# Kernel tuning notes

Hardware: AMD Instinct MI355X
Metric: run time of the kernel (lower is better)

The kernel has to match this reference:

```python
import jax, jax.numpy as jnp
import numpy as np

C = 256
LN_EPS = 1e-5

def setup_inputs() -> dict:
    key = jax.random.key(0)
    ks = jax.random.split(key, 12)
    B, M, N = 8, 4096, 4096
    scale = 1.0 / np.sqrt(C)
    inp = {
        'x': jax.random.normal(ks[0], (B, M, C), jnp.float32),
        'y': jax.random.normal(ks[1], (B, N, C), jnp.float32),
        'Wq': jax.random.normal(ks[2], (C, C), jnp.float32) * scale,
        'bq': jnp.zeros((C,), jnp.float32),
        'Wk': jax.random.normal(ks[3], (C, C), jnp.float32) * scale,
        'bk': jnp.zeros((C,), jnp.float32),
        'Wv': jax.random.normal(ks[4], (C, C), jnp.float32) * scale,
        'bv': jnp.zeros((C,), jnp.float32),
        'Wo': jax.random.normal(ks[5], (C, C), jnp.float32) * (scale * 1e-5),
        'bo': jnp.zeros((C,), jnp.float32),
        'gamma': jnp.ones((C,), jnp.float32),
        'beta': jnp.zeros((C,), jnp.float32),
    }
    return inp

def reference(x, y, Wq, bq, Wk, bk, Wv, bv, Wo, bo, gamma, beta):
    # projections (torch Linear: x @ W.T + b)
    q = x @ Wq.T + bq                      # [B,M,C]
    k = y @ Wk.T + bk                      # [B,N,C]
    v = y @ Wv.T + bv                      # [B,N,C]
    # scaled dot-product attention with explicit score matrix
    w = jnp.einsum('bmc,bnc->bmn', q, k) * (C ** -0.5)  # [B,M,N]
    w = jax.nn.softmax(w, axis=-1)
    h = jnp.einsum('bmn,bnc->bmc', w, v)   # [B,M,C]
    h = h @ Wo.T + bo
    z = x + h
    # LayerNorm over last dim
    mu = jnp.mean(z, axis=-1, keepdims=True)
    var = jnp.var(z, axis=-1, keepdims=True)
    out = (z - mu) * jax.lax.rsqrt(var + LN_EPS) * gamma + beta
    return out
```

## Files before the change

kernel.cpp:

```cpp
#include <hip/hip_runtime.h>
#include <hip/hip_bf16.h>

#define C_DIM 256
#define QSCALE 0.09016844f
#define WO_SCALE 1048576.0f
#define WO_INV   9.5367431640625e-07f

typedef __attribute__((ext_vector_type(8))) short bf16x8;
typedef __attribute__((ext_vector_type(4))) float f32x4;
typedef __attribute__((ext_vector_type(16))) float f32x16;

__device__ __forceinline__ void gload16(const unsigned char* g, unsigned char* l) {
    __builtin_amdgcn_global_load_lds(
        (const __attribute__((address_space(1))) void*)g,
        (__attribute__((address_space(3))) void*)l, 16, 0, 0);
}

__global__ void cvt_w_kernel(const float* __restrict__ w0, const float* __restrict__ w1,
                             const float* __restrict__ w2, const float* __restrict__ w3,
                             unsigned char* __restrict__ o0, unsigned char* __restrict__ o1,
                             unsigned char* __restrict__ o2, unsigned char* __restrict__ o3) {
    int i = (blockIdx.x * 256 + threadIdx.x) * 4;
    #pragma unroll
    for (int wsel = 0; wsel < 4; ++wsel) {
        const float* w = wsel == 0 ? w0 : (wsel == 1 ? w1 : (wsel == 2 ? w2 : w3));
        unsigned char* o = wsel == 0 ? o0 : (wsel == 1 ? o1 : (wsel == 2 ? o2 : o3));
        const float sc = (wsel == 3) ? WO_SCALE : 1.0f;
        float4 v = *reinterpret_cast<const float4*>(w + i);
        unsigned p = __builtin_amdgcn_cvt_pk_fp8_f32(v.x * sc, v.y * sc, 0, false);
        p = __builtin_amdgcn_cvt_pk_fp8_f32(v.z * sc, v.w * sc, p, true);
        *reinterpret_cast<unsigned*>(o + i) = p;
    }
}

__global__ __launch_bounds__(256, 1)
void proj_kernel(const float* __restrict__ x, const float* __restrict__ y,
                 const unsigned char* __restrict__ wq8, const unsigned char* __restrict__ wk8,
                 const unsigned char* __restrict__ wv8,
                 const float* __restrict__ bqp, const float* __restrict__ bkp,
                 const float* __restrict__ bvp,
                 unsigned char* __restrict__ qo, unsigned char* __restrict__ ko,
                 unsigned char* __restrict__ vo)
{
    __shared__ __align__(16) unsigned char ldsW[65536];
    __shared__ __align__(16) unsigned char ldsA[32768];

    const int which = blockIdx.x >> 8;
    const int tile = blockIdx.x & 255;
    const float* in = (which == 0) ? x : y;
    const unsigned char* wsrc = (which == 0) ? wq8 : (which == 1 ? wk8 : wv8);
    const float* bias = (which == 0) ? bqp : (which == 1 ? bkp : bvp);
    unsigned char* out = (which == 0) ? qo : (which == 1 ? ko : vo);
    const float oscale = (which == 0) ? QSCALE : 1.0f;

    const int tid = threadIdx.x;
    const int rowbase = tile * 128;

    #pragma unroll
    for (int it = 0; it < 16; ++it) {
        int G = it * 256 + tid;
        int c = G >> 4, p = G & 15;
        gload16(wsrc + c * 256 + ((p ^ (c & 15)) << 4), ldsW + G * 16);
    }
    #pragma unroll
    for (int it = 0; it < 32; ++it) {
        int e = it * 1024 + tid * 4;
        int r = e >> 8, c4 = e & 255;
        float4 v = *reinterpret_cast<const float4*>(in + (size_t)(rowbase + r) * C_DIM + c4);
        unsigned p = __builtin_amdgcn_cvt_pk_fp8_f32(v.x, v.y, 0, false);
        p = __builtin_amdgcn_cvt_pk_fp8_f32(v.z, v.w, p, true);
        int g = (c4 >> 4) ^ (r & 15);
        *reinterpret_cast<unsigned*>(ldsA + r * 256 + g * 16 + (c4 & 12)) = p;
    }
    __syncthreads();

    const int lane = tid & 63, wave = tid >> 6;
    const int lrow = lane & 15, lkq = lane >> 4;
    const int koff = (lkq & 1) << 3;
    const int kg = lkq >> 1;

    #pragma unroll
    for (int ms = 0; ms < 2; ++ms) {
        const int arow = wave * 32 + ms * 16 + lrow;
        long a[8];
        #pragma unroll
        for (int ks = 0; ks < 8; ++ks)
            a[ks] = *reinterpret_cast<const long*>(
                ldsA + arow * 256 + (((ks * 2 + kg) ^ (arow & 15)) << 4) + koff);

        f32x4 acc[16];
        #pragma unroll
        for (int nf = 0; nf < 16; ++nf) acc[nf] = f32x4{0.f, 0.f, 0.f, 0.f};

        #pragma unroll
        for (int nf = 0; nf < 16; ++nf) {
            const int c = nf * 16 + lrow;
            const unsigned char* wb = ldsW + c * 256;
            const int cx = c & 15;
            #pragma unroll
            for (int ks = 0; ks < 8; ++ks) {
                long b = *reinterpret_cast<const long*>(wb + (((ks * 2 + kg) ^ cx) << 4) + koff);
                acc[nf] = __builtin_amdgcn_mfma_f32_16x16x32_fp8_fp8(a[ks], b, acc[nf], 0, 0, 0);
            }
        }

        const int base = rowbase + wave * 32 + ms * 16 + lkq * 4;
        if (which != 2) {
            const int rsw = (which == 1) ? (base & 8) : 0;
            #pragma unroll
            for (int nf = 0; nf < 16; ++nf) {
                float bv = bias[nf * 16 + lrow];
                float v0 = (acc[nf][0] + bv) * oscale, v1 = (acc[nf][1] + bv) * oscale;
                float v2 = (acc[nf][2] + bv) * oscale, v3 = (acc[nf][3] + bv) * oscale;
                unsigned p = __builtin_amdgcn_cvt_pk_fp8_f32(v0, v1, 0, false);
                p = __builtin_amdgcn_cvt_pk_fp8_f32(v2, v3, p, true);
                int col = (nf * 16 + lrow) ^ rsw;
                unsigned char* o = out + (size_t)base * C_DIM + col;
                o[0]   = (unsigned char)p;
                o[256] = (unsigned char)(p >> 8);
                o[512] = (unsigned char)(p >> 16);
                o[768] = (unsigned char)(p >> 24);
            }
        } else {
            int bb = base >> 12, n0 = base & 4095;
            #pragma unroll
            for (int nf = 0; nf < 16; ++nf) {
                float bv = bias[nf * 16 + lrow];
                float v0 = acc[nf][0] + bv, v1 = acc[nf][1] + bv;
                float v2 = acc[nf][2] + bv, v3 = acc[nf][3] + bv;
                unsigned p = __builtin_amdgcn_cvt_pk_fp8_f32(v0, v1, 0, false);
                p = __builtin_amdgcn_cvt_pk_fp8_f32(v2, v3, p, true);
                int c = nf * 16 + lrow;
                *reinterpret_cast<unsigned*>(vo + ((size_t)bb * C_DIM + c) * 4096 + (n0 ^ (c & 8))) = p;
            }
        }
    }
}

__global__ __launch_bounds__(512, 1)
void attn_kernel(const unsigned char* __restrict__ qg, const unsigned char* __restrict__ kg,
                 const unsigned char* __restrict__ vtg, unsigned short* __restrict__ hg)
{
    __shared__ __align__(16) unsigned short smem[65536];
    unsigned char* smb = (unsigned char*)smem;

    const int tid = threadIdx.x;
    const int lane = tid & 63;
    const int w = tid >> 6;
    const int wq = w & 3;
    const int half = w >> 2;
    const int l31 = lane & 31;
    const int hi5 = lane >> 5;
    const int ksw = l31 & 15;
    const int hsw = ((l31 >> 3) & 1) << 3;
    const int vsw = ((l31 >> 2) & 1);

    const int batch = blockIdx.x & 7;
    const int mt = blockIdx.x >> 3;
    const size_t q0 = (size_t)batch * 4096 + mt * 128 + wq * 32;

    const unsigned char* kbase = kg + ((size_t)batch * 4096 + half * 2048) * 256;
    const unsigned char* vbase = vtg + (size_t)batch * 256 * 4096 + half * 2048;

    long qf[16];
    #pragma unroll
    for (int ks = 0; ks < 16; ++ks)
        qf[ks] = *reinterpret_cast<const long*>(qg + (q0 + l31) * 256 + ks * 16 + hi5 * 8);

    f32x16 o[8];
    #pragma unroll
    for (int cb = 0; cb < 8; ++cb) {
        #pragma unroll
        for (int r = 0; r < 16; ++r) o[cb][r] = 0.f;
    }

    float m_run = -__builtin_inff();
    float lsum = 0.f;

    auto stage = [&](int buf, int kt) {
        const int kv0 = kt * 32;
        unsigned char* lk = smb + (half * 2 + buf) * 8192;
        unsigned char* lv = smb + 32768 + (half * 2 + buf) * 8192;
        #pragma unroll
        for (int i = 0; i < 2; ++i) {
            int g = wq * 128 + i * 64 + lane;
            int row = g >> 4, pos = g & 15;
            gload16(kbase + (size_t)(kv0 + row) * 256 + ((pos ^ (row & 15)) << 4), lk + g * 16);
        }
        #pragma unroll
        for (int i = 0; i < 2; ++i) {
            int s = wq * 128 + i * 64 + lane;
            int c = s >> 1;
            int k2 = (s & 1) ^ ((s >> 3) & 1);
            gload16(vbase + (size_t)c * 4096 + kv0 + k2 * 16, lv + s * 16);
        }
    };

    stage(0, 0);
    __syncthreads();

    for (int kt = 0; kt < 64; ++kt) {
        const int cur = kt & 1;
        if (kt < 63) stage(cur ^ 1, kt + 1);

        const unsigned char* kc = smb + (half * 2 + cur) * 8192;
        const unsigned char* vc = smb + 32768 + (half * 2 + cur) * 8192;

        f32x16 s0;
        #pragma unroll
        for (int r = 0; r < 16; ++r) s0[r] = 0.f;
        const unsigned char* krow = kc + l31 * 256 + ((hi5 * 8) ^ hsw);
        __builtin_amdgcn_s_setprio(1);
        #pragma unroll
        for (int ks = 0; ks < 16; ++ks) {
            long a0 = *reinterpret_cast<const long*>(krow + ((ks ^ ksw) << 4));
            s0 = __builtin_amdgcn_mfma_f32_32x32x16_fp8_fp8(a0, qf[ks], s0, 0, 0, 0);
        }
        __builtin_amdgcn_s_setprio(0);

        float mloc = s0[0];
        #pragma unroll
        for (int r = 1; r < 16; ++r) mloc = fmaxf(mloc, s0[r]);
        mloc = fmaxf(mloc, __shfl_xor(mloc, 32, 64));

        if (__any(mloc > m_run + 8.0f)) {
            float mn = fmaxf(m_run, mloc);
            float al = exp2f(m_run - mn);
            m_run = mn;
            lsum *= al;
            #pragma unroll
            for (int cb = 0; cb < 8; ++cb) {
                #pragma unroll
                for (int r = 0; r < 16; ++r) o[cb][r] *= al;
            }
        }

        float ts = 0.f;
        #pragma unroll
        for (int r = 0; r < 16; ++r) { s0[r] = exp2f(s0[r] - m_run); ts += s0[r]; }
        ts += __shfl_xor(ts, 32, 64);
        lsum += ts;

        unsigned Wu[8];
        #pragma unroll
        for (int a = 0; a < 8; ++a) {
            unsigned p = __builtin_amdgcn_cvt_pk_fp8_f32(s0[4 * a], s0[4 * a + 1], 0, false);
            Wu[a] = __builtin_amdgcn_cvt_pk_fp8_f32(s0[4 * a + 2], s0[4 * a + 3], p, true);
        }

        const bool h = (hi5 != 0);
        const unsigned char* vrow = vc + l31 * 32 + ((hi5 * 8) ^ hsw);
        __builtin_amdgcn_s_setprio(1);
        #pragma unroll
        for (int ksv = 0; ksv < 2; ++ksv) {
            unsigned snd = h ? Wu[2 * ksv] : Wu[2 * ksv + 1];
            unsigned rcv = __shfl_xor(snd, 32, 64);
            unsigned wlo = h ? rcv : Wu[2 * ksv];
            unsigned whi = h ? Wu[2 * ksv + 1] : rcv;
            long pb = (long)(((unsigned long long)whi << 32) | (unsigned long long)wlo);
            const int k2s = (ksv ^ vsw) << 4;
            #pragma unroll
            for (int cb = 0; cb < 8; ++cb) {
                long vf = *reinterpret_cast<const long*>(vrow + cb * 1024 + k2s);
                o[cb] = __builtin_amdgcn_mfma_f32_32x32x16_fp8_fp8(vf, pb, o[cb], 0, 0, 0);
            }
        }
        __builtin_amdgcn_s_setprio(0);

        __syncthreads();
    }

    float* sf = (float*)smem;

    if (half == 1 && hi5 == 0) {
        sf[(wq * 32 + l31) * 2]     = m_run;
        sf[(wq * 32 + l31) * 2 + 1] = lsum;
    }
    __syncthreads();

    float m1 = 0.f, l1 = 0.f;
    if (half == 0) {
        m1 = sf[(wq * 32 + l31) * 2];
        l1 = sf[(wq * 32 + l31) * 2 + 1];
    }
    __syncthreads();

    if (half == 1) {
        #pragma unroll
        for (int cb = 0; cb < 8; ++cb) {
            #pragma unroll
            for (int r = 0; r < 16; ++r) {
                int c = cb * 32 + (r & 3) + 8 * (r >> 2) + 4 * hi5;
                sf[wq * 8192 + c * 32 + l31] = o[cb][r];
            }
        }
    }
    __syncthreads();

    if (half == 0) {
        float mm = fmaxf(m_run, m1);
        float a0 = exp2f(m_run - mm), a1 = exp2f(m1 - mm);
        float lt = lsum * a0 + l1 * a1;
        float rinv = 1.0f / lt;
        float f0 = a0 * rinv, f1 = a1 * rinv;

        unsigned short* tr = smem + wq * 16384;
        #pragma unroll
        for (int cc = 0; cc < 4; ++cc) {
            #pragma unroll
            for (int cbh = 0; cbh < 2; ++cbh) {
                const int cb = cc * 2 + cbh;
                #pragma unroll
                for (int rp = 0; rp < 8; ++rp) {
                    const int r = 2 * rp;
                    int c_lo = cb * 32 + (r & 3) + 8 * (r >> 2) + 4 * hi5;
                    float v_lo = o[cb][r]     * f0 + sf[wq * 8192 + c_lo * 32 + l31]       * f1;
                    float v_hi = o[cb][r + 1] * f0 + sf[wq * 8192 + (c_lo + 1) * 32 + l31] * f1;
                    unsigned wpk;
                    asm("v_cvt_pk_bf16_f32 %0, %1, %2" : "=v"(wpk) : "v"(v_lo), "v"(v_hi));
                    int c_local = 32 * cbh + (r & 3) + 8 * (r >> 2) + 4 * hi5;
                    *reinterpret_cast<unsigned*>(tr + l31 * 72 + c_local) = wpk;
                }
            }
            __builtin_amdgcn_s_waitcnt(0);
            #pragma unroll
            for (int i = 0; i < 4; ++i) {
                int idx = i * 64 + lane;
                int q = idx >> 3, ch = idx & 7;
                uint4 d = *reinterpret_cast<const uint4*>(tr + q * 72 + ch * 8);
                *reinterpret_cast<uint4*>(hg + (q0 + q) * 256 + cc * 64 + ch * 8) = d;
            }
        }
    }
}

__global__ __launch_bounds__(256, 1)
void out_kernel(const unsigned short* __restrict__ hb, const unsigned char* __restrict__ wo8,
                const float* __restrict__ bo, const float* __restrict__ xg,
                const float* __restrict__ gamma, const float* __restrict__ beta,
                float* __restrict__ outg)
{
    __shared__ __align__(16) unsigned char ldsW[65536];
    __shared__ __align__(16) unsigned char ldsA[32768];

    const int tid = threadIdx.x;
    const int rowbase = blockIdx.x * 128;

    #pragma unroll
    for (int it = 0; it < 16; ++it) {
        int G = it * 256 + tid;
        int c = G >> 4, p = G & 15;
        gload16(wo8 + c * 256 + ((p ^ (c & 15)) << 4), ldsW + G * 16);
    }
    #pragma unroll
    for (int it = 0; it < 16; ++it) {
        int e = it * 2048 + tid * 8;
        int r = e >> 8, c8 = e & 255;
        uint4 d = *reinterpret_cast<const uint4*>(hb + (size_t)(rowbase + r) * C_DIM + c8);
        union { unsigned u; float f; } f0, f1, f2, f3, f4, f5, f6, f7;
        f0.u = d.x << 16; f1.u = d.x & 0xffff0000u;
        f2.u = d.y << 16; f3.u = d.y & 0xffff0000u;
        f4.u = d.z << 16; f5.u = d.z & 0xffff0000u;
        f6.u = d.w << 16; f7.u = d.w & 0xffff0000u;
        unsigned p0 = __builtin_amdgcn_cvt_pk_fp8_f32(f0.f, f1.f, 0, false);
        p0 = __builtin_amdgcn_cvt_pk_fp8_f32(f2.f, f3.f, p0, true);
        unsigned p1 = __builtin_amdgcn_cvt_pk_fp8_f32(f4.f, f5.f, 0, false);
        p1 = __builtin_amdgcn_cvt_pk_fp8_f32(f6.f, f7.f, p1, true);
        int g = (c8 >> 4) ^ (r & 15);
        uint2 pk; pk.x = p0; pk.y = p1;
        *reinterpret_cast<uint2*>(ldsA + r * 256 + g * 16 + (c8 & 8)) = pk;
    }
    __syncthreads();

    const int lane = tid & 63, wave = tid >> 6;
    const int lrow = lane & 15, lkq = lane >> 4;
    const int koff = (lkq & 1) << 3;
    const int kg = lkq >> 1;

    #pragma unroll
    for (int ms = 0; ms < 2; ++ms) {
        const int arow = wave * 32 + ms * 16 + lrow;
        long a[8];
        #pragma unroll
        for (int ks = 0; ks < 8; ++ks)
            a[ks] = *reinterpret_cast<const long*>(
                ldsA + arow * 256 + (((ks * 2 + kg) ^ (arow & 15)) << 4) + koff);

        f32x4 acc[16];
        #pragma unroll
        for (int nf = 0; nf < 16; ++nf) acc[nf] = f32x4{0.f, 0.f, 0.f, 0.f};

        #pragma unroll
        for (int nf = 0; nf < 16; ++nf) {
            const int c = nf * 16 + lrow;
            const unsigned char* wb = ldsW + c * 256;
            const int cx = c & 15;
            #pragma unroll
            for (int ks = 0; ks < 8; ++ks) {
                long b = *reinterpret_cast<const long*>(wb + (((ks * 2 + kg) ^ cx) << 4) + koff);
                acc[nf] = __builtin_amdgcn_mfma_f32_16x16x32_fp8_fp8(a[ks], b, acc[nf], 0, 0, 0);
            }
        }

        const int base = rowbase + wave * 32 + ms * 16 + lkq * 4;

        #pragma unroll
        for (int nf = 0; nf < 16; ++nf) {
            float bv = bo[nf * 16 + lrow];
            #pragma unroll
            for (int r = 0; r < 4; ++r) {
                size_t row = base + r;
                acc[nf][r] = acc[nf][r] * WO_INV + bv + xg[row * C_DIM + nf * 16 + lrow];
            }
        }

        float mu[4], rstd[4];
        #pragma unroll
        for (int r = 0; r < 4; ++r) {
            float s1 = 0.f, s2 = 0.f;
            #pragma unroll
            for (int nf = 0; nf < 16; ++nf) { float v = acc[nf][r]; s1 += v; s2 += v * v; }
            #pragma unroll
            for (int off = 1; off < 16; off <<= 1) {
                s1 += __shfl_xor(s1, off, 64);
                s2 += __shfl_xor(s2, off, 64);
            }
            float m = s1 * (1.f / 256.f);
            mu[r] = m;
            rstd[r] = rsqrtf(s2 * (1.f / 256.f) - m * m + 1e-5f);
        }

        #pragma unroll
        for (int nf = 0; nf < 16; ++nf) {
            float g = gamma[nf * 16 + lrow];
            float bt = beta[nf * 16 + lrow];
            #pragma unroll
            for (int r = 0; r < 4; ++r) {
                size_t row = base + r;
                outg[row * C_DIM + nf * 16 + lrow] = (acc[nf][r] - mu[r]) * rstd[r] * g + bt;
            }
        }
    }
}

extern "C" void kernel_launch(void* const* d_in, const int* in_sizes, int n_in,
                              void* d_out, int out_size, void* d_ws, size_t ws_size,
                              hipStream_t stream) {
    const float* x     = (const float*)d_in[0];
    const float* y     = (const float*)d_in[1];
    const float* Wq    = (const float*)d_in[2];
    const float* bq    = (const float*)d_in[3];
    const float* Wk    = (const float*)d_in[4];
    const float* bk    = (const float*)d_in[5];
    const float* Wv    = (const float*)d_in[6];
    const float* bv    = (const float*)d_in[7];
    const float* Wo    = (const float*)d_in[8];
    const float* bo    = (const float*)d_in[9];
    const float* gamma = (const float*)d_in[10];
    const float* beta  = (const float*)d_in[11];
    float* out = (float*)d_out;

    unsigned char* ws = (unsigned char*)d_ws;
    unsigned char* wq8 = ws;
    unsigned char* wk8 = ws + 65536;
    unsigned char* wv8 = ws + 131072;
    unsigned char* wo8 = ws + 196608;
    unsigned char* q_b = ws + 262144;
    unsigned char* k_b = q_b + 8388608;
    unsigned char* v_b = k_b + 8388608;
    unsigned short* h_b = (unsigned short*)(v_b + 8388608);

    cvt_w_kernel<<<64, 256, 0, stream>>>(Wq, Wk, Wv, Wo, wq8, wk8, wv8, wo8);

    proj_kernel<<<768, 256, 0, stream>>>(x, y, wq8, wk8, wv8, bq, bk, bv, q_b, k_b, v_b);

    attn_kernel<<<256, 512, 0, stream>>>(q_b, k_b, v_b, h_b);

    out_kernel<<<256, 256, 0, stream>>>(h_b, wo8, bo, x, gamma, beta, out);
}
```

Baseline: 184.6 us.

## Skew softmax/PV phase in second wave group and triple-buffer V tiles

The KV-split attention kernel now runs a software-pipelined schedule in the second half of the waves: each iteration does the softmax and PV for the previous tile before the QK^T MFMAs for the current tile. The aim is to stagger the two halves so their MFMA and VALU/exp phases overlap on the SIMDs. V gets three LDS buffers to support the one-tile lag, which grows shared memory to 96KB. The cross-half partial output is now passed through LDS as swizzled bf16 instead of fp32, cutting LDS traffic at the cost of some precision in the merge.

```diff
diff --git a/kernel.cpp b/kernel.cpp
--- a/kernel.cpp
+++ b/kernel.cpp
@@ -141,8 +141,7 @@
 void attn_kernel(const unsigned char* __restrict__ qg, const unsigned char* __restrict__ kg,
                  const unsigned char* __restrict__ vtg, unsigned short* __restrict__ hg)
 {
-    __shared__ __align__(16) unsigned short smem[65536];
-    unsigned char* smb = (unsigned char*)smem;
+    __shared__ __align__(16) unsigned char smb[98304];
 
     const int tid = threadIdx.x;
     const int lane = tid & 63;
@@ -177,10 +176,10 @@
     float m_run = -__builtin_inff();
     float lsum = 0.f;
 
-    auto stage = [&](int buf, int kt) {
+    auto stage = [&](int kb, int vb, int kt) {
         const int kv0 = kt * 32;
-        unsigned char* lk = smb + (half * 2 + buf) * 8192;
-        unsigned char* lv = smb + 32768 + (half * 2 + buf) * 8192;
+        unsigned char* lk = smb + (half * 2 + kb) * 8192;
+        unsigned char* lv = smb + 32768 + (half * 3 + vb) * 8192;
         #pragma unroll
         for (int i = 0; i < 2; ++i) {
             int g = wq * 128 + i * 64 + lane;
@@ -196,31 +195,23 @@
         }
     };
 
-    stage(0, 0);
-    __syncthreads();
-
-    for (int kt = 0; kt < 64; ++kt) {
-        const int cur = kt & 1;
-        if (kt < 63) stage(cur ^ 1, kt + 1);
-
-        const unsigned char* kc = smb + (half * 2 + cur) * 8192;
-        const unsigned char* vc = smb + 32768 + (half * 2 + cur) * 8192;
-
-        f32x16 s0;
-        #pragma unroll
-        for (int r = 0; r < 16; ++r) s0[r] = 0.f;
-        const unsigned char* krow = kc + l31 * 256 + ((hi5 * 8) ^ hsw);
+    auto do_S = [&](int kb, f32x16& sreg) {
+        const unsigned char* krow = smb + (half * 2 + kb) * 8192 + l31 * 256 + ((hi5 * 8) ^ hsw);
+        #pragma unroll
+        for (int r = 0; r < 16; ++r) sreg[r] = 0.f;
         __builtin_amdgcn_s_setprio(1);
         #pragma unroll
         for (int ks = 0; ks < 16; ++ks) {
             long a0 = *reinterpret_cast<const long*>(krow + ((ks ^ ksw) << 4));
-            s0 = __builtin_amdgcn_mfma_f32_32x32x16_fp8_fp8(a0, qf[ks], s0, 0, 0, 0);
+            sreg = __builtin_amdgcn_mfma_f32_32x32x16_fp8_fp8(a0, qf[ks], sreg, 0, 0, 0);
         }
         __builtin_amdgcn_s_setprio(0);
-
-        float mloc = s0[0];
-        #pragma unroll
-        for (int r = 1; r < 16; ++r) mloc = fmaxf(mloc, s0[r]);
+    };
+
+    auto do_SMPV = [&](f32x16& sreg, int vb) {
+        float mloc = sreg[0];
+        #pragma unroll
+        for (int r = 1; r < 16; ++r) mloc = fmaxf(mloc, sreg[r]);
         mloc = fmaxf(mloc, __shfl_xor(mloc, 32, 64));
 
         if (__any(mloc > m_run + 8.0f)) {
@@ -237,19 +228,20 @@
 
         float ts = 0.f;
         #pragma unroll
-        for (int r = 0; r < 16; ++r) { s0[r] = exp2f(s0[r] - m_run); ts += s0[r]; }
+        for (int r = 0; r < 16; ++r) { sreg[r] = exp2f(sreg[r] - m_run); ts += sreg[r]; }
         ts += __shfl_xor(ts, 32, 64);
         lsum += ts;
 
         unsigned Wu[8];
         #pragma unroll
         for (int a = 0; a < 8; ++a) {
-            unsigned p = __builtin_amdgcn_cvt_pk_fp8_f32(s0[4 * a], s0[4 * a + 1], 0, false);
-            Wu[a] = __builtin_amdgcn_cvt_pk_fp8_f32(s0[4 * a + 2], s0[4 * a + 3], p, true);
+            unsigned p = __builtin_amdgcn_cvt_pk_fp8_f32(sreg[4 * a], sreg[4 * a + 1], 0, false);
+            Wu[a] = __builtin_amdgcn_cvt_pk_fp8_f32(sreg[4 * a + 2], sreg[4 * a + 3], p, true);
         }
 
         const bool h = (hi5 != 0);
-        const unsigned char* vrow = vc + l31 * 32 + ((hi5 * 8) ^ hsw);
+        const unsigned char* vrow = smb + 32768 + (half * 3 + vb) * 8192
+                                    + l31 * 32 + ((hi5 * 8) ^ hsw);
         __builtin_amdgcn_s_setprio(1);
         #pragma unroll
         for (int ksv = 0; ksv < 2; ++ksv) {
@@ -266,45 +258,72 @@
             }
         }
         __builtin_amdgcn_s_setprio(0);
-
-        __syncthreads();
-    }
-
-    float* sf = (float*)smem;
-
-    if (half == 1 && hi5 == 0) {
-        sf[(wq * 32 + l31) * 2]     = m_run;
-        sf[(wq * 32 + l31) * 2 + 1] = lsum;
-    }
+    };
+
+    stage(0, 0, 0);
     __syncthreads();
 
-    float m1 = 0.f, l1 = 0.f;
+    f32x16 s0;
     if (half == 0) {
-        m1 = sf[(wq * 32 + l31) * 2];
-        l1 = sf[(wq * 32 + l31) * 2 + 1];
-    }
+        int vcur = 0, vnxt = 1;
+        for (int kt = 0; kt < 64; ++kt) {
+            if (kt < 63) stage((kt + 1) & 1, vnxt, kt + 1);
+            do_S(kt & 1, s0);
+            do_SMPV(s0, vcur);
+            __syncthreads();
+            vcur = vnxt; vnxt = (vnxt == 2) ? 0 : vnxt + 1;
+        }
+    } else {
+        int vprv = 2, vcur = 0, vnxt = 1;
+        for (int kt = 0; kt < 64; ++kt) {
+            if (kt < 63) stage((kt + 1) & 1, vnxt, kt + 1);
+            if (kt > 0) do_SMPV(s0, vprv);
+            do_S(kt & 1, s0);
+            __syncthreads();
+            vprv = vcur; vcur = vnxt; vnxt = (vnxt == 2) ? 0 : vnxt + 1;
+        }
+        do_SMPV(s0, vprv);
+    }
+
     __syncthreads();
 
+    unsigned short* pub = (unsigned short*)smb;
+    float* ml = (float*)(smb + 90112);
+
     if (half == 1) {
+        if (hi5 == 0) {
+            ml[(wq * 32 + l31) * 2]     = m_run;
+            ml[(wq * 32 + l31) * 2 + 1] = lsum;
+        }
+        unsigned short* prow = pub + (wq * 32 + l31) * 256;
+        const int cxor = (l31 & 15) << 2;
         #pragma unroll
         for (int cb = 0; cb < 8; ++cb) {
             #pragma unroll
-            for (int r = 0; r < 16; ++r) {
+            for (int rp = 0; rp < 8; ++rp) {
+                const int r = 2 * rp;
+                unsigned wpk;
+                float lo = o[cb][r], hi_ = o[cb][r + 1];
+                asm("v_cvt_pk_bf16_f32 %0, %1, %2" : "=v"(wpk) : "v"(lo), "v"(hi_));
                 int c = cb * 32 + (r & 3) + 8 * (r >> 2) + 4 * hi5;
-                sf[wq * 8192 + c * 32 + l31] = o[cb][r];
+                *reinterpret_cast<unsigned*>(prow + (c ^ cxor)) = wpk;
             }
         }
     }
     __syncthreads();
 
     if (half == 0) {
+        float m1 = ml[(wq * 32 + l31) * 2];
+        float l1 = ml[(wq * 32 + l31) * 2 + 1];
         float mm = fmaxf(m_run, m1);
         float a0 = exp2f(m_run - mm), a1 = exp2f(m1 - mm);
         float lt = lsum * a0 + l1 * a1;
         float rinv = 1.0f / lt;
         float f0 = a0 * rinv, f1 = a1 * rinv;
 
-        unsigned short* tr = smem + wq * 16384;
+        const unsigned short* prow = pub + (wq * 32 + l31) * 256;
+        const int cxor = (l31 & 15) << 2;
+        unsigned short* tr = (unsigned short*)(smb + 65536 + wq * 4608);
         #pragma unroll
         for (int cc = 0; cc < 4; ++cc) {
             #pragma unroll
@@ -313,9 +332,12 @@
                 #pragma unroll
                 for (int rp = 0; rp < 8; ++rp) {
                     const int r = 2 * rp;
-                    int c_lo = cb * 32 + (r & 3) + 8 * (r >> 2) + 4 * hi5;
-                    float v_lo = o[cb][r]     * f0 + sf[wq * 8192 + c_lo * 32 + l31]       * f1;
-                    float v_hi = o[cb][r + 1] * f0 + sf[wq * 8192 + (c_lo + 1) * 32 + l31] * f1;
+                    int c = cb * 32 + (r & 3) + 8 * (r >> 2) + 4 * hi5;
+                    unsigned pk = *reinterpret_cast<const unsigned*>(prow + (c ^ cxor));
+                    union { unsigned u; float f; } b0, b1;
+                    b0.u = pk << 16; b1.u = pk & 0xffff0000u;
+                    float v_lo = o[cb][r]     * f0 + b0.f * f1;
+                    float v_hi = o[cb][r + 1] * f0 + b1.f * f1;
                     unsigned wpk;
                     asm("v_cvt_pk_bf16_f32 %0, %1, %2" : "=v"(wpk) : "v"(v_lo), "v"(v_hi));
                     int c_local = 32 * cbh + (r & 3) + 8 * (r >> 2) + 4 * hi5;
```

Result: slower. 196.3 us (+6.3%).

## Split attention columns across waves with rotating single-wave softmax via LDS

Applied to the files above, without the earlier changes.

Reworks the attention kernel so each 256-thread block owns 32 query rows and each wave owns a 64-column slice of the output. One wave per KV tile, chosen round-robin, computes scores and the online softmax, then writes P and the rescale factors to LDS for all waves to use in the PV MFMAs. This cuts accumulator registers per wave, allowing four blocks per CU and removing the two-half merge at the end. In exchange, the score/softmax stage is serialized on one wave per tile and two block barriers are added per tile.

```diff
diff --git a/kernel.cpp b/kernel.cpp
--- a/kernel.cpp
+++ b/kernel.cpp
@@ -137,18 +137,15 @@
     }
 }
 
-__global__ __launch_bounds__(512, 1)
+__global__ __launch_bounds__(256, 4)
 void attn_kernel(const unsigned char* __restrict__ qg, const unsigned char* __restrict__ kg,
                  const unsigned char* __restrict__ vtg, unsigned short* __restrict__ hg)
 {
-    __shared__ __align__(16) unsigned short smem[65536];
-    unsigned char* smb = (unsigned char*)smem;
+    __shared__ __align__(16) unsigned char smb[35584];
 
     const int tid = threadIdx.x;
     const int lane = tid & 63;
     const int w = tid >> 6;
-    const int wq = w & 3;
-    const int half = w >> 2;
     const int l31 = lane & 31;
     const int hi5 = lane >> 5;
     const int ksw = l31 & 15;
@@ -157,39 +154,33 @@
 
     const int batch = blockIdx.x & 7;
     const int mt = blockIdx.x >> 3;
-    const size_t q0 = (size_t)batch * 4096 + mt * 128 + wq * 32;
-
-    const unsigned char* kbase = kg + ((size_t)batch * 4096 + half * 2048) * 256;
-    const unsigned char* vbase = vtg + (size_t)batch * 256 * 4096 + half * 2048;
+    const size_t q0 = (size_t)batch * 4096 + mt * 32;
+
+    const unsigned char* kbase = kg + (size_t)batch * 4096 * 256;
+    const unsigned char* vbase = vtg + (size_t)batch * 256 * 4096;
 
     long qf[16];
     #pragma unroll
     for (int ks = 0; ks < 16; ++ks)
         qf[ks] = *reinterpret_cast<const long*>(qg + (q0 + l31) * 256 + ks * 16 + hi5 * 8);
 
-    f32x16 o[8];
-    #pragma unroll
-    for (int cb = 0; cb < 8; ++cb) {
-        #pragma unroll
-        for (int r = 0; r < 16; ++r) o[cb][r] = 0.f;
-    }
-
-    float m_run = -__builtin_inff();
-    float lsum = 0.f;
+    f32x16 o0, o1;
+    #pragma unroll
+    for (int r = 0; r < 16; ++r) { o0[r] = 0.f; o1[r] = 0.f; }
 
     auto stage = [&](int buf, int kt) {
         const int kv0 = kt * 32;
-        unsigned char* lk = smb + (half * 2 + buf) * 8192;
-        unsigned char* lv = smb + 32768 + (half * 2 + buf) * 8192;
+        unsigned char* lk = smb + buf * 8192;
+        unsigned char* lv = smb + 16384 + buf * 8192;
         #pragma unroll
         for (int i = 0; i < 2; ++i) {
-            int g = wq * 128 + i * 64 + lane;
+            int g = w * 128 + i * 64 + lane;
             int row = g >> 4, pos = g & 15;
             gload16(kbase + (size_t)(kv0 + row) * 256 + ((pos ^ (row & 15)) << 4), lk + g * 16);
         }
         #pragma unroll
         for (int i = 0; i < 2; ++i) {
-            int s = wq * 128 + i * 64 + lane;
+            int s = w * 128 + i * 64 + lane;
             int c = s >> 1;
             int k2 = (s & 1) ^ ((s >> 3) & 1);
             gload16(vbase + (size_t)c * 4096 + kv0 + k2 * 16, lv + s * 16);
@@ -199,138 +190,124 @@
     stage(0, 0);
     __syncthreads();
 
-    for (int kt = 0; kt < 64; ++kt) {
+    for (int kt = 0; kt < 128; ++kt) {
         const int cur = kt & 1;
-        if (kt < 63) stage(cur ^ 1, kt + 1);
-
-        const unsigned char* kc = smb + (half * 2 + cur) * 8192;
-        const unsigned char* vc = smb + 32768 + (half * 2 + cur) * 8192;
-
-        f32x16 s0;
-        #pragma unroll
-        for (int r = 0; r < 16; ++r) s0[r] = 0.f;
-        const unsigned char* krow = kc + l31 * 256 + ((hi5 * 8) ^ hsw);
-        __builtin_amdgcn_s_setprio(1);
-        #pragma unroll
-        for (int ks = 0; ks < 16; ++ks) {
-            long a0 = *reinterpret_cast<const long*>(krow + ((ks ^ ksw) << 4));
-            s0 = __builtin_amdgcn_mfma_f32_32x32x16_fp8_fp8(a0, qf[ks], s0, 0, 0, 0);
-        }
-        __builtin_amdgcn_s_setprio(0);
-
-        float mloc = s0[0];
-        #pragma unroll
-        for (int r = 1; r < 16; ++r) mloc = fmaxf(mloc, s0[r]);
-        mloc = fmaxf(mloc, __shfl_xor(mloc, 32, 64));
-
-        if (__any(mloc > m_run + 8.0f)) {
-            float mn = fmaxf(m_run, mloc);
-            float al = exp2f(m_run - mn);
-            m_run = mn;
-            lsum *= al;
-            #pragma unroll
-            for (int cb = 0; cb < 8; ++cb) {
-                #pragma unroll
-                for (int r = 0; r < 16; ++r) o[cb][r] *= al;
-            }
-        }
-
-        float ts = 0.f;
-        #pragma unroll
-        for (int r = 0; r < 16; ++r) { s0[r] = exp2f(s0[r] - m_run); ts += s0[r]; }
-        ts += __shfl_xor(ts, 32, 64);
-        lsum += ts;
-
-        unsigned Wu[8];
-        #pragma unroll
-        for (int a = 0; a < 8; ++a) {
-            unsigned p = __builtin_amdgcn_cvt_pk_fp8_f32(s0[4 * a], s0[4 * a + 1], 0, false);
-            Wu[a] = __builtin_amdgcn_cvt_pk_fp8_f32(s0[4 * a + 2], s0[4 * a + 3], p, true);
-        }
-
-        const bool h = (hi5 != 0);
-        const unsigned char* vrow = vc + l31 * 32 + ((hi5 * 8) ^ hsw);
-        __builtin_amdgcn_s_setprio(1);
-        #pragma unroll
-        for (int ksv = 0; ksv < 2; ++ksv) {
-            unsigned snd = h ? Wu[2 * ksv] : Wu[2 * ksv + 1];
-            unsigned rcv = __shfl_xor(snd, 32, 64);
-            unsigned wlo = h ? rcv : Wu[2 * ksv];
-            unsigned whi = h ? Wu[2 * ksv + 1] : rcv;
-            long pb = (long)(((unsigned long long)whi << 32) | (unsigned long long)wlo);
-            const int k2s = (ksv ^ vsw) << 4;
-            #pragma unroll
-            for (int cb = 0; cb < 8; ++cb) {
-                long vf = *reinterpret_cast<const long*>(vrow + cb * 1024 + k2s);
-                o[cb] = __builtin_amdgcn_mfma_f32_32x32x16_fp8_fp8(vf, pb, o[cb], 0, 0, 0);
-            }
-        }
-        __builtin_amdgcn_s_setprio(0);
-
+        if (kt < 127) stage(cur ^ 1, kt + 1);
+
+        if (w == (kt & 3)) {
+            f32x16 s0;
+            #pragma unroll
+            for (int r = 0; r < 16; ++r) s0[r] = 0.f;
+            const unsigned char* krow = smb + cur * 8192 + l31 * 256 + ((hi5 * 8) ^ hsw);
+            __builtin_amdgcn_s_setprio(1);
+            #pragma unroll
+            for (int ks = 0; ks < 16; ++ks) {
+                long a0 = *reinterpret_cast<const long*>(krow + ((ks ^ ksw) << 4));
+                s0 = __builtin_amdgcn_mfma_f32_32x32x16_fp8_fp8(a0, qf[ks], s0, 0, 0, 0);
+            }
+            __builtin_amdgcn_s_setprio(0);
+
+            float mloc = s0[0];
+            #pragma unroll
+            for (int r = 1; r < 16; ++r) mloc = fmaxf(mloc, s0[r]);
+            mloc = fmaxf(mloc, __shfl_xor(mloc, 32, 64));
+
+            float m_prev, l_prev;
+            if (kt == 0) { m_prev = -__builtin_inff(); l_prev = 0.f; }
+            else {
+                const float* Mp = reinterpret_cast<const float*>(smb + 34816 + ((kt - 1) & 1) * 384);
+                m_prev = Mp[32 + l31];
+                l_prev = Mp[64 + l31];
+            }
+            float alpha = 1.0f, m_new = m_prev;
+            if (__any(mloc > m_prev + 8.0f)) {
+                m_new = fmaxf(m_prev, mloc);
+                alpha = exp2f(m_prev - m_new);
+            }
+            float ts = 0.f;
+            #pragma unroll
+            for (int r = 0; r < 16; ++r) { s0[r] = exp2f(s0[r] - m_new); ts += s0[r]; }
+            ts += __shfl_xor(ts, 32, 64);
+            float l_new = l_prev * alpha + ts;
+
+            unsigned Wu[4];
+            #pragma unroll
+            for (int a = 0; a < 4; ++a) {
+                unsigned p = __builtin_amdgcn_cvt_pk_fp8_f32(s0[4 * a], s0[4 * a + 1], 0, false);
+                Wu[a] = __builtin_amdgcn_cvt_pk_fp8_f32(s0[4 * a + 2], s0[4 * a + 3], p, true);
+            }
+            const bool h = (hi5 != 0);
+            long pb0 = 0, pb1 = 0;
+            #pragma unroll
+            for (int ksv = 0; ksv < 2; ++ksv) {
+                unsigned snd = h ? Wu[2 * ksv] : Wu[2 * ksv + 1];
+                unsigned rcv = __shfl_xor(snd, 32, 64);
+                unsigned wlo = h ? rcv : Wu[2 * ksv];
+                unsigned whi = h ? Wu[2 * ksv + 1] : rcv;
+                long pb = (long)(((unsigned long long)whi << 32) | (unsigned long long)wlo);
+                if (ksv == 0) pb0 = pb; else pb1 = pb;
+            }
+
+            union { long l[2]; uint4 u; } pw;
+            pw.l[0] = pb0; pw.l[1] = pb1;
+            *reinterpret_cast<uint4*>(smb + 32768 + cur * 1024 + lane * 16) = pw.u;
+            if (hi5 == 0) {
+                float* Mc = reinterpret_cast<float*>(smb + 34816 + cur * 384);
+                Mc[l31]      = alpha;
+                Mc[32 + l31] = m_new;
+                Mc[64 + l31] = l_new;
+            }
+        }
         __syncthreads();
-    }
-
-    float* sf = (float*)smem;
-
-    if (half == 1 && hi5 == 0) {
-        sf[(wq * 32 + l31) * 2]     = m_run;
-        sf[(wq * 32 + l31) * 2 + 1] = lsum;
-    }
-    __syncthreads();
-
-    float m1 = 0.f, l1 = 0.f;
-    if (half == 0) {
-        m1 = sf[(wq * 32 + l31) * 2];
-        l1 = sf[(wq * 32 + l31) * 2 + 1];
-    }
-    __syncthreads();
-
-    if (half == 1) {
-        #pragma unroll
-        for (int cb = 0; cb < 8; ++cb) {
-            #pragma unroll
-            for (int r = 0; r < 16; ++r) {
-                int c = cb * 32 + (r & 3) + 8 * (r >> 2) + 4 * hi5;
-                sf[wq * 8192 + c * 32 + l31] = o[cb][r];
-            }
-        }
-    }
-    __syncthreads();
-
-    if (half == 0) {
-        float mm = fmaxf(m_run, m1);
-        float a0 = exp2f(m_run - mm), a1 = exp2f(m1 - mm);
-        float lt = lsum * a0 + l1 * a1;
-        float rinv = 1.0f / lt;
-        float f0 = a0 * rinv, f1 = a1 * rinv;
-
-        unsigned short* tr = smem + wq * 16384;
-        #pragma unroll
-        for (int cc = 0; cc < 4; ++cc) {
-            #pragma unroll
-            for (int cbh = 0; cbh < 2; ++cbh) {
-                const int cb = cc * 2 + cbh;
-                #pragma unroll
-                for (int rp = 0; rp < 8; ++rp) {
-                    const int r = 2 * rp;
-                    int c_lo = cb * 32 + (r & 3) + 8 * (r >> 2) + 4 * hi5;
-                    float v_lo = o[cb][r]     * f0 + sf[wq * 8192 + c_lo * 32 + l31]       * f1;
-                    float v_hi = o[cb][r + 1] * f0 + sf[wq * 8192 + (c_lo + 1) * 32 + l31] * f1;
-                    unsigned wpk;
-                    asm("v_cvt_pk_bf16_f32 %0, %1, %2" : "=v"(wpk) : "v"(v_lo), "v"(v_hi));
-                    int c_local = 32 * cbh + (r & 3) + 8 * (r >> 2) + 4 * hi5;
-                    *reinterpret_cast<unsigned*>(tr + l31 * 72 + c_local) = wpk;
-                }
-            }
-            __builtin_amdgcn_s_waitcnt(0);
-            #pragma unroll
-            for (int i = 0; i < 4; ++i) {
-                int idx = i * 64 + lane;
-                int q = idx >> 3, ch = idx & 7;
-                uint4 d = *reinterpret_cast<const uint4*>(tr + q * 72 + ch * 8);
-                *reinterpret_cast<uint4*>(hg + (q0 + q) * 256 + cc * 64 + ch * 8) = d;
-            }
-        }
+
+        {
+            const float* Mc = reinterpret_cast<const float*>(smb + 34816 + cur * 384);
+            float alpha = Mc[l31];
+            #pragma unroll
+            for (int r = 0; r < 16; ++r) { o0[r] *= alpha; o1[r] *= alpha; }
+
+            uint4 pq = *reinterpret_cast<const uint4*>(smb + 32768 + cur * 1024 + lane * 16);
+            long pb0 = (long)(((unsigned long long)pq.y << 32) | (unsigned long long)pq.x);
+            long pb1 = (long)(((unsigned long long)pq.w << 32) | (unsigned long long)pq.z);
+
+            const unsigned char* vrow = smb + 16384 + cur * 8192 + l31 * 32 + ((hi5 * 8) ^ hsw);
+            __builtin_amdgcn_s_setprio(1);
+            #pragma unroll
+            for (int ksv = 0; ksv < 2; ++ksv) {
+                const int k2s = (ksv ^ vsw) << 4;
+                long vf0 = *reinterpret_cast<const long*>(vrow + (w * 2 + 0) * 1024 + k2s);
+                o0 = __builtin_amdgcn_mfma_f32_32x32x16_fp8_fp8(vf0, ksv ? pb1 : pb0, o0, 0, 0, 0);
+                long vf1 = *reinterpret_cast<const long*>(vrow + (w * 2 + 1) * 1024 + k2s);
+                o1 = __builtin_amdgcn_mfma_f32_32x32x16_fp8_fp8(vf1, ksv ? pb1 : pb0, o1, 0, 0, 0);
+            }
+            __builtin_amdgcn_s_setprio(0);
+        }
+        __syncthreads();
+    }
+
+    float rinv = 1.0f / reinterpret_cast<const float*>(smb + 34816 + 384)[64 + l31];
+
+    unsigned short* tr = reinterpret_cast<unsigned short*>(smb + w * 4608);
+    #pragma unroll
+    for (int rp = 0; rp < 8; ++rp) {
+        const int r = 2 * rp;
+        const int cl = (r & 3) + 8 * (r >> 2) + 4 * hi5;
+        float a0 = o0[r] * rinv, a1 = o0[r + 1] * rinv;
+        unsigned w0;
+        asm("v_cvt_pk_bf16_f32 %0, %1, %2" : "=v"(w0) : "v"(a0), "v"(a1));
+        *reinterpret_cast<unsigned*>(tr + l31 * 72 + cl) = w0;
+        float b0 = o1[r] * rinv, b1 = o1[r + 1] * rinv;
+        unsigned w1;
+        asm("v_cvt_pk_bf16_f32 %0, %1, %2" : "=v"(w1) : "v"(b0), "v"(b1));
+        *reinterpret_cast<unsigned*>(tr + l31 * 72 + 32 + cl) = w1;
+    }
+    __builtin_amdgcn_s_waitcnt(0);
+    #pragma unroll
+    for (int i = 0; i < 4; ++i) {
+        int idx = i * 64 + lane;
+        int q = idx >> 3, ch = idx & 7;
+        uint4 d = *reinterpret_cast<const uint4*>(tr + q * 72 + ch * 8);
+        *reinterpret_cast<uint4*>(hg + (q0 + q) * 256 + w * 64 + ch * 8) = d;
     }
 }
 
@@ -474,7 +451,7 @@
 
     proj_kernel<<<768, 256, 0, stream>>>(x, y, wq8, wk8, wv8, bq, bk, bv, q_b, k_b, v_b);
 
-    attn_kernel<<<256, 512, 0, stream>>>(q_b, k_b, v_b, h_b);
+    attn_kernel<<<1024, 256, 0, stream>>>(q_b, k_b, v_b, h_b);
 
     out_kernel<<<256, 256, 0, stream>>>(h_b, wo8, bo, x, gamma, beta, out);
 }
```

After: 308.8 us. 1.67x slower.
